# Performance work log

Hardware: AMD Instinct MI355X
Metric: run time of the kernel (lower is better)

The kernel has to match this reference:

```python
import jax, jax.numpy as jnp
import numpy as np

B, N, NODE_DIM, D, H, K, VP = 64, 1024, 8, 128, 4, 16, 128
FF = 512


def _layernorm(x, g, b):
    m = jnp.mean(x, axis=-1, keepdims=True)
    v = jnp.var(x, axis=-1, keepdims=True)
    return (x - m) * jax.lax.rsqrt(v + 1e-5) * g + b


def setup_inputs() -> dict:
    key = jax.random.key(0)
    kit = iter(jax.random.split(key, 64))

    def w(*shape):
        fan_in = shape[-2] if len(shape) >= 2 else shape[-1]
        return jax.random.normal(next(kit), shape, jnp.float32) / np.sqrt(fan_in)

    return dict(
        node_inputs=jax.random.normal(next(kit), (B, N, NODE_DIM), jnp.float32),
        node_padding_mask=jnp.zeros((B, 1, N), jnp.bool_),
        current_index=jax.random.randint(next(kit), (B, 1, 1), 0, N),
        viewpoints=jax.random.randint(next(kit), (B, VP, 1), 0, N),
        viewpoint_padding_mask=jnp.zeros((B, 1, VP), jnp.bool_),
        adj_list=jax.random.randint(next(kit), (B, N, K), 0, N),
        W_init=w(NODE_DIM, D), b_init=jnp.zeros((D,), jnp.float32),
        gcn_W=w(4, D, D), gcn_b=jnp.zeros((4, D), jnp.float32),
        tc_fc_W=w(D, D), tc_fc_b=jnp.zeros((D,), jnp.float32),
        tc_ln1_g=jnp.ones((D,), jnp.float32), tc_ln1_b=jnp.zeros((D,), jnp.float32),
        Wq=w(D, H * D), bq=jnp.zeros((H * D,), jnp.float32),
        Wk=w(D, H * D), bk=jnp.zeros((H * D,), jnp.float32),
        Wv=w(D, H * D), bv=jnp.zeros((H * D,), jnp.float32),
        tc_ln2_g=jnp.ones((D,), jnp.float32), tc_ln2_b=jnp.zeros((D,), jnp.float32),
        sg_fc_W=w(D, D), sg_fc_b=jnp.zeros((D,), jnp.float32),
        dec_Wq=w(D, D), dec_Wk=w(D, D), dec_Wv=w(D, D), dec_Wo=w(D, D),
        dec_ln1_g=jnp.ones((D,), jnp.float32), dec_ln1_b=jnp.zeros((D,), jnp.float32),
        ff_W1=w(D, FF), ff_b1=jnp.zeros((FF,), jnp.float32),
        ff_W2=w(FF, D), ff_b2=jnp.zeros((D,), jnp.float32),
        dec_ln2_g=jnp.ones((D,), jnp.float32), dec_ln2_b=jnp.zeros((D,), jnp.float32),
        q_W=w(3 * D, 1), q_b=jnp.zeros((1,), jnp.float32),
    )


def _forward(node_inputs, node_padding_mask, current_index, viewpoints, viewpoint_padding_mask, adj_list,
             W_init, b_init, gcn_W, gcn_b, tc_fc_W, tc_fc_b, tc_ln1_g, tc_ln1_b,
             Wq, bq, Wk, bk, Wv, bv, tc_ln2_g, tc_ln2_b, sg_fc_W, sg_fc_b,
             dec_Wq, dec_Wk, dec_Wv, dec_Wo, dec_ln1_g, dec_ln1_b,
             ff_W1, ff_b1, ff_W2, ff_b2, dec_ln2_g, dec_ln2_b, q_W, q_b):
    Bb, Nn, nd = node_inputs.shape
    d = W_init.shape[1]
    nH = Wq.shape[1] // d  # SGFormer attention heads (per-head dim = d)
    BN = Bb * Nn
    # ---- initial embedding + batched block-diagonal sparse edges (prepare_batch_data) ----
    x0 = node_inputs.reshape(BN, nd) @ W_init + b_init
    offset = (jnp.arange(Bb) * Nn)[:, None, None]
    valid = adj_list >= 0
    row = (jnp.broadcast_to(jnp.arange(Nn)[None, :, None], adj_list.shape) + offset).reshape(-1)
    col = (jnp.where(valid, adj_list, 0) + offset).reshape(-1)
    ew = valid.reshape(-1).astype(x0.dtype)
    deg = jax.ops.segment_sum(ew, row, num_segments=BN) + 1.0  # +1 self-loop
    dinv = jax.lax.rsqrt(deg)
    enorm = (dinv[row] * dinv[col] * ew)[:, None]

    def gcn_conv(h, W, b):
        hw = h @ W
        agg = jax.ops.segment_sum(enorm * hw[col], row, num_segments=BN)
        return agg + hw / deg[:, None] + b  # self-loop term D^-1 * x W

    h = x0
    n_layers = gcn_W.shape[0]
    for i in range(n_layers):
        h = gcn_conv(h, gcn_W[i], gcn_b[i])
        if i < n_layers - 1:
            h = jax.nn.relu(h)
    gnn_out = h
    # ---- SGFormer TransConv: fc -> LN -> relu, then linear global attention over all BN nodes ----
    z0 = jax.nn.relu(_layernorm(x0 @ tc_fc_W + tc_fc_b, tc_ln1_g, tc_ln1_b))
    q = (z0 @ Wq + bq).reshape(BN, nH, d)
    k = (z0 @ Wk + bk).reshape(BN, nH, d)
    v = (z0 @ Wv + bv).reshape(BN, nH, d)
    qs = q / jnp.linalg.norm(q)  # global Frobenius norm, as in SGFormer
    ks = k / jnp.linalg.norm(k)
    Nf = jnp.asarray(BN, x0.dtype)
    kvs = jnp.einsum('lhm,lhd->hmd', ks, v)
    num = jnp.einsum('nhm,hmd->nhd', qs, kvs) + Nf * v
    den = jnp.einsum('nhm,hm->nh', qs, ks.sum(axis=0))[..., None] + Nf
    attn = (num / den).mean(axis=1)  # mean over heads -> [BN, d]
    z = jax.nn.relu(_layernorm(0.5 * attn + 0.5 * z0, tc_ln2_g, tc_ln2_b))  # alpha=0.5 residual
    enhanced = ((0.8 * gnn_out + 0.2 * z) @ sg_fc_W + sg_fc_b).reshape(Bb, Nn, d)  # graph_weight=0.8
    # ---- decoder: gather current node, masked cross-attention to all nodes ----
    cur = jnp.take_along_axis(enhanced, jnp.broadcast_to(current_index, (Bb, 1, d)), axis=1)
    dH = 4
    dk = d // dH
    qd = (cur @ dec_Wq).reshape(Bb, 1, dH, dk).transpose(0, 2, 1, 3)
    kd = (enhanced @ dec_Wk).reshape(Bb, Nn, dH, dk).transpose(0, 2, 1, 3)
    vd = (enhanced @ dec_Wv).reshape(Bb, Nn, dH, dk).transpose(0, 2, 1, 3)
    scores = jnp.einsum('bhqe,bhne->bhqn', qd, kd) / np.sqrt(dk).astype(np.float32)
    scores = jnp.where(node_padding_mask[:, None, :, :], -1e9, scores)
    wts = jax.nn.softmax(scores, axis=-1)
    att = jnp.einsum('bhqn,bhne->bhqe', wts, vd).transpose(0, 2, 1, 3).reshape(Bb, 1, d) @ dec_Wo
    t = _layernorm(cur + att, dec_ln1_g, dec_ln1_b)
    glob = _layernorm(t + jax.nn.relu(t @ ff_W1 + ff_b1) @ ff_W2 + ff_b2, dec_ln2_g, dec_ln2_b)
    # ---- Q head: gather viewpoints, concat(global, current, viewpoint) -> Linear(3d, 1) ----
    Vp = viewpoints.shape[1]
    vp = jnp.take_along_axis(enhanced, jnp.broadcast_to(viewpoints, (Bb, Vp, d)), axis=1)
    cs = jnp.concatenate([glob, cur], axis=-1)  # [B,1,2d]
    af = jnp.concatenate([jnp.broadcast_to(cs, (Bb, Vp, 2 * d)), vp], axis=-1)
    return af @ q_W + q_b  # [B, Vp, 1]


def reference(node_inputs, node_padding_mask, current_index, viewpoints, viewpoint_padding_mask, adj_list,
              W_init, b_init, gcn_W, gcn_b, tc_fc_W, tc_fc_b, tc_ln1_g, tc_ln1_b,
              Wq, bq, Wk, bk, Wv, bv, tc_ln2_g, tc_ln2_b, sg_fc_W, sg_fc_b,
              dec_Wq, dec_Wk, dec_Wv, dec_Wo, dec_ln1_g, dec_ln1_b,
              ff_W1, ff_b1, ff_W2, ff_b2, dec_ln2_g, dec_ln2_b, q_W, q_b):
    return _forward(node_inputs, node_padding_mask, current_index, viewpoints, viewpoint_padding_mask, adj_list,
                    W_init, b_init, gcn_W, gcn_b, tc_fc_W, tc_fc_b, tc_ln1_g, tc_ln1_b,
                    Wq, bq, Wk, bk, Wv, bv, tc_ln2_g, tc_ln2_b, sg_fc_W, sg_fc_b,
                    dec_Wq, dec_Wk, dec_Wv, dec_Wo, dec_ln1_g, dec_ln1_b,
                    ff_W1, ff_b1, ff_W2, ff_b2, dec_ln2_g, dec_ln2_b, q_W, q_b)
```

## Files before the change

### kernel.cpp

```cpp
#include <hip/hip_runtime.h>

#define BNn 65536L

typedef unsigned short u16;
typedef unsigned int u32;
typedef __attribute__((ext_vector_type(8))) short short8;
typedef __attribute__((ext_vector_type(4))) float f32x4;

__device__ inline u16 f2b(float f){ u32 u = __float_as_uint(f); u32 r = (u + 0x7fffu + ((u>>16)&1u))>>16; return (u16)r; }
__device__ inline float b2f(u16 b){ return __uint_as_float(((u32)b)<<16); }

__global__ __launch_bounds__(256) void k_init(const float* __restrict__ gcnW, const float* __restrict__ tcW,
                       const float* __restrict__ sgW, const float* __restrict__ dKW,
                       const float* __restrict__ dVW,
                       const float* __restrict__ Wq, const float* __restrict__ Wk, const float* __restrict__ Wv,
                       const float* __restrict__ in, const float* __restrict__ Wi, const float* __restrict__ bi,
                       const int* __restrict__ adj, float* __restrict__ dinv,
                       u16* __restrict__ wts, float* __restrict__ SqSkz, u16* __restrict__ x0) {
  __shared__ u16 sT[64 * 136];
  __shared__ float Ws[1024];
  __shared__ float bs[128];
  __shared__ float ins[256];
  int bid = blockIdx.x, t = threadIdx.x;
  if (bid < 41) {
// ... 185 lines not shown
      int valid = a >= 0;
      int cc = (valid ? a : 0) + bb;
      cols[q] = cc;
      enq[q] = valid ? din * dinv[cc] : 0.0f;
    }
    float acc[32];
    {
      const u16* hr = h + n * 128 + seg * 32;
      uint4 v0 = *(const uint4*)(hr), v1 = *(const uint4*)(hr + 8), v2 = *(const uint4*)(hr + 16), v3 = *(const uint4*)(hr + 24);
      const u16* pv = (const u16*)&v0;
#pragma unroll
      for (int i = 0; i < 8; i++) acc[i] = b2f(pv[i]) * d2v;
      pv = (const u16*)&v1;
#pragma unroll
      for (int i = 0; i < 8; i++) acc[8 + i] = b2f(pv[i]) * d2v;
      pv = (const u16*)&v2;
#pragma unroll
      for (int i = 0; i < 8; i++) acc[16 + i] = b2f(pv[i]) * d2v;
      pv = (const u16*)&v3;
#pragma unroll
      for (int i = 0; i < 8; i++) acc[24 + i] = b2f(pv[i]) * d2v;
    }
#pragma unroll
    for (int j = 0; j < 16; j++) {
      int src = (lane & 60) | (j >> 2);
      int cc = __shfl(cols[j & 3], src);
      float e = __shfl(enq[j & 3], src);
      const u16* nb = h + (long)cc * 128 + seg * 32;
      uint4 v0 = *(const uint4*)(nb), v1 = *(const uint4*)(nb + 8), v2 = *(const uint4*)(nb + 16), v3 = *(const uint4*)(nb + 24);
      const u16* pv = (const u16*)&v0;
#pragma unroll
      for (int i = 0; i < 8; i++) acc[i] += e * b2f(pv[i]);
      pv = (const u16*)&v1;
#pragma unroll
      for (int i = 0; i < 8; i++) acc[8 + i] += e * b2f(pv[i]);
      pv = (const u16*)&v2;
#pragma unroll
      for (int i = 0; i < 8; i++) acc[16 + i] += e * b2f(pv[i]);
      pv = (const u16*)&v3;
#pragma unroll
      for (int i = 0; i < 8; i++) acc[24 + i] += e * b2f(pv[i]);
    }
    u16 ob[32];
#pragma unroll
    for (int i = 0; i < 32; i++) ob[i] = f2b(acc[i]);
    uint4* o4 = (uint4*)(sA + row * 132 + seg * 32);
    uint4* s4 = (uint4*)ob;
#pragma unroll
    for (int i = 0; i < 4; i++) o4[i] = s4[i];
  }
  __syncthreads();
  int wave = t >> 6, m = lane & 15, g = lane >> 4;
  const u16* aB = sA + (wave * 16 + m) * 132 + g * 8;
  short8 a[4];
#pragma unroll
  for (int s = 0; s < 4; s++) a[s] = *(const short8*)(aB + s * 32);
  f32x4 acc[8];
#pragma unroll
  for (int c = 0; c < 8; c++) {
    float bc = gb[c * 16 + m];
    acc[c] = (f32x4){bc, bc, bc, bc};
  }
#pragma unroll
  for (int s = 0; s < 4; s++) {
#pragma unroll
    for (int c = 0; c < 8; c++) {
      short8 bb = *(const short8*)(sW + (c * 16 + m) * 132 + g * 8 + s * 32);
      acc[c] = __builtin_amdgcn_mfma_f32_16x16x32_bf16(a[s], bb, acc[c], 0, 0, 0);
    }
  }
#pragma unroll
  for (int c = 0; c < 8; c++) {
    int col = c * 16 + m;
#pragma unroll
    for (int r = 0; r < 4; r++) {
      float y = acc[c][r];
      if (relu) y = fmaxf(y, 0.f);
      out[(n0 + wave * 16 + g * 4 + r) * 128 + col] = f2b(y);
    }
  }
}

__global__ __launch_bounds__(256) void k_gram(const u16* __restrict__ z0T,
                                              float* __restrict__ Gpart, float* __restrict__ zsum) {
  __shared__ u16 sZT[128 * 264];
  int t = threadIdx.x;
  int wave = t >> 6, lane = t & 63, m = lane & 15, g = lane >> 4;
  f32x4 acc[2][8];
#pragma unroll
  for (int i = 0; i < 2; i++)
#pragma unroll
    for (int c = 0; c < 8; c++) acc[i][c] = (f32x4){0.f, 0.f, 0.f, 0.f};
  float zs = 0.f;
  for (int sl = 0; sl < 2; sl++) {
    long k0 = (long)(blockIdx.x * 2 + sl) * 256;
    __syncthreads();
#pragma unroll
    for (int i = 0; i < 16; i++) {
      int idx = t + i * 256; int mm = idx >> 5, ch = idx & 31;
      *(float4*)(sZT + mm * 264 + ch * 8) = *(const float4*)(z0T + (long)mm * BNn + k0 + ch * 8);
    }
    __syncthreads();
#pragma unroll
    for (int kk = 0; kk < 8; kk++) {
      short8 a0 = *(const short8*)(sZT + (wave * 32 + m) * 264 + kk * 32 + g * 8);
      short8 a1 = *(const short8*)(sZT + (wave * 32 + 16 + m) * 264 + kk * 32 + g * 8);
#pragma unroll
      for (int c = 0; c < 8; c++) {
        short8 bb = *(const short8*)(sZT + (c * 16 + m) * 264 + kk * 32 + g * 8);
        acc[0][c] = __builtin_amdgcn_mfma_f32_16x16x32_bf16(a0, bb, acc[0][c], 0, 0, 0);
        acc[1][c] = __builtin_amdgcn_mfma_f32_16x16x32_bf16(a1, bb, acc[1][c], 0, 0, 0);
      }
    }
    if (t < 128) {
      float s = 0.f;
      for (int j = 0; j < 256; j++) s += b2f(sZT[t * 264 + j]);
      zs += s;
    }
  }
  if (t < 128) atomicAdd(&zsum[t], zs);
  float* P = Gpart + (long)blockIdx.x * 16384 + wave * 4096;
#pragma unroll
  for (int i = 0; i < 2; i++)
#pragma unroll
    for (int c = 0; c < 8; c++)
      *(f32x4*)(P + (i * 8 + c) * 256 + lane * 4) = acc[i][c];
}

__global__ void k_gram_red(const float* __restrict__ Gpart, float* __restrict__ G) {
  int o = blockIdx.x * 256 + threadIdx.x;
  float s = 0.f;
  for (int b = 0; b < 128; b++) s += Gpart[(long)b * 16384 + o];
  int wave = o >> 12, rem = o & 4095;
  int ic = rem >> 8, i = ic >> 3, c = ic & 7;
  int rem2 = rem & 255, lane = rem2 >> 2, q = rem2 & 3;
  int m = lane & 15, g = lane >> 4;
  int mi = wave * 32 + i * 16 + g * 4 + q;
  int mj = c * 16 + m;
  G[mi * 128 + mj] = s;
}

__global__ __launch_bounds__(256) void k_statskvs(const float* __restrict__ Wq, const float* __restrict__ bq,
                                                  const float* __restrict__ Wk, const float* __restrict__ bk,
                                                  const float* __restrict__ Wv, const float* __restrict__ bv,
                                                  const float* __restrict__ G, const float* __restrict__ zsum,
                                                  float* __restrict__ ksum,
                                                  float* __restrict__ Sq, float* __restrict__ Sk,
                                                  u16* __restrict__ kvsT) {
  int t = threadIdx.x;
  int blk = blockIdx.x;
  if (blk < 2) {
    int c = blk * 256 + t;
    float s = 0.f;
    for (int i = 0; i < 128; i++) s += Wk[i * 512 + c] * zsum[i];
    ksum[c] = s + 65536.0f * bk[c];
    return;
  }
  if (blk < 130) {
    __shared__ float wcol[128];
    __shared__ float red[256];
    int bi = blk - 2;
    int isK = bi >> 6;
    const float* W = isK ? Wk : Wq;
    const float* bb = isK ? bk : bq;
    float* S = isK ? Sk : Sq;
    int c0 = (bi & 63) * 8;
    float tot = 0.f;
    for (int cc = 0; cc < 8; cc++) {
      int c = c0 + cc;
      __syncthreads();
      if (t < 128) wcol[t] = W[t * 512 + c];
      __syncthreads();
      float v = 0.f;
      if (t < 128) {
        float uu = 0.f;
        for (int j = 0; j < 128; j++) uu += G[t * 128 + j] * wcol[j];
        v = uu * wcol[t] + 2.0f * bb[c] * wcol[t] * zsum[t];
      }
      red[t] = v;
      __syncthreads();
      for (int o = 128; o > 0; o >>= 1) { if (t < o) red[t] += red[t + o]; __syncthreads(); }
      if (t == 0) tot += red[0] + 65536.0f * bb[c] * bb[c];
    }
    if (t == 0) atomicAdd(S, tot);
    return;
  }
  {
    __shared__ float wv8[128][8];
    __shared__ float U[128][8];
    __shared__ float zv[8];
    int bi = blk - 130;
    int h = bi >> 4, dg = bi & 15;
    if (t < 128) {
#pragma unroll
      for (int dd = 0; dd < 8; dd++) wv8[t][dd] = Wv[t * 512 + h * 128 + dg * 8 + dd];
    }
    __syncthreads();
    {
      int i = t & 127, du = t >> 7;
      float a0 = 0.f, a1 = 0.f, a2 = 0.f, a3 = 0.f;
      for (int j = 0; j < 128; j++) {
        float gg = G[i * 128 + j];
        a0 += gg * wv8[j][du * 4 + 0]; a1 += gg * wv8[j][du * 4 + 1];
        a2 += gg * wv8[j][du * 4 + 2]; a3 += gg * wv8[j][du * 4 + 3];
      }
      U[i][du * 4 + 0] = a0; U[i][du * 4 + 1] = a1; U[i][du * 4 + 2] = a2; U[i][du * 4 + 3] = a3;
    }
    if (t < 8) {
      float s = 0.f;
      for (int i = 0; i < 128; i++) s += zsum[i] * wv8[i][t];
      zv[t] = s;
    }
    __syncthreads();
    {
      int m = t & 127, du = t >> 7;
      int colk = h * 128 + m;
      float bkm = bk[colk];
      float a[4] = {0.f, 0.f, 0.f, 0.f};
      float wkzs = 0.f;
      for (int i = 0; i < 128; i++) {
        float wk = Wk[i * 512 + colk];
        wkzs += wk * zsum[i];
#pragma unroll
        for (int q = 0; q < 4; q++) a[q] += wk * U[i][du * 4 + q];
      }
#pragma unroll
      for (int q = 0; q < 4; q++) {
        int dd = du * 4 + q;
        int cold = h * 128 + dg * 8 + dd;
        float val = a[q] + wkzs * bv[cold] + bkm * zv[dd] + 65536.0f * bkm * bv[cold];
        kvsT[h * 16384 + (dg * 8 + dd) * 128 + m] = f2b(val);
      }
    }
  }
}

__global__ __launch_bounds__(256) void k_prepB(const float* __restrict__ Wq, const float* __restrict__ bq,
                                               const float* __restrict__ Wv, const float* __restrict__ bv,
                                               const u16* __restrict__ kvsT, const float* __restrict__ ksum,
                                               const float* __restrict__ SqSk,
                                               u16* __restrict__ Bmat, float* __restrict__ cAv,
                                               u16* __restrict__ U16, float* __restrict__ consts) {
  __shared__ float kvr[8][128];
  int t = threadIdx.x;
  int h = blockIdx.x >> 4, dg = blockIdx.x & 15;
  float inv = rsqrtf(SqSk[0] * SqSk[1]);
  for (int i = t; i < 1024; i += 256) {
    int dl = i >> 7, m = i & 127;
    kvr[dl][m] = b2f(kvsT[h * 16384 + (dg * 8 + dl) * 128 + m]);
  }
  __syncthreads();
  {
    int k = t & 127, du = t >> 7;
    const float* wqr = Wq + k * 512 + h * 128;
    float acc[4] = {0.f, 0.f, 0.f, 0.f};
    for (int m = 0; m < 128; m++) {
      float w = wqr[m];
#pragma unroll
      for (int q = 0; q < 4; q++) acc[q] += w * kvr[du * 4 + q][m];
    }
#pragma unroll
    for (int q = 0; q < 4; q++) {
      int dd = dg * 8 + du * 4 + q;
      float mv = acc[q] * inv + 65536.0f * Wv[k * 512 + h * 128 + dd];
      Bmat[((long)h * 128 + dd) * 128 + k] = f2b(mv);
    }
  }
  if (t < 8) {
    float s = 0.f;
    for (int m = 0; m < 128; m++) s += bq[h * 128 + m] * kvr[t][m];
    cAv[h * 128 + dg * 8 + t] = s * inv + 65536.0f * bv[h * 128 + dg * 8 + t];
  }
  if (dg == 0) {
    if (t < 128) {
      float s = 0.f;
      for (int m = 0; m < 128; m++) s += Wq[t * 512 + h * 128 + m] * ksum[h * 128 + m];
      U16[h * 128 + t] = f2b(s * inv);
    } else if (t == 128) {
      float s = 0.f;
      for (int m = 0; m < 128; m++) s += bq[h * 128 + m] * ksum[h * 128 + m];
      consts[h] = s * inv + 65536.0f;
    }
    if (h == 0) {
      for (int i = t; i < 1536; i += 256) U16[512 + i] = 0;
    }
  }
}

__global__ __launch_bounds__(512) void k_numfuse(const u16* __restrict__ z0, const u16* __restrict__ gnn,
                                                 const u16* __restrict__ Bmat,
                                                 const float* __restrict__ cAv, const u16* __restrict__ U16,
                                                 const float* __restrict__ consts,
                                                 const float* __restrict__ g2, const float* __restrict__ b2,
                                                 const u16* __restrict__ wsg, const float* __restrict__ sgb,
                                                 u16* __restrict__ enh) {
  __shared__ u16 sA[128 * 132];
  __shared__ u16 sB[128 * 132];
  __shared__ float rden[512];
  __shared__ float caL[512];
  int t = threadIdx.x;
  long n0 = (long)blockIdx.x * 128;
  int wave = t >> 6, lane = t & 63, m = lane & 15, g = lane >> 4;
  u16* myA = sA + wave * 16 * 132;
  {
    const u16* zg = z0 + (n0 + wave * 16) * 128;
#pragma unroll
    for (int i = 0; i < 4; i++) {
      int idx = lane + i * 64; int row = idx >> 4, ch = idx & 15;
      *(float4*)(myA + row * 132 + ch * 8) = *(const float4*)(zg + row * 128 + ch * 8);
    }
  }
  caL[t] = cAv[t & 511];
  const u16* aB = sA + (wave * 16 + m) * 132 + g * 8;
  short8 a[4];
#pragma unroll
  for (int s = 0; s < 4; s++) a[s] = *(const short8*)(aB + s * 32);
  {
    f32x4 accd = (f32x4){0.f, 0.f, 0.f, 0.f};
#pragma unroll
    for (int s = 0; s < 4; s++) {
      short8 ub = *(const short8*)(U16 + m * 128 + g * 8 + s * 32);
      accd = __builtin_amdgcn_mfma_f32_16x16x32_bf16(a[s], ub, accd, 0, 0, 0);
    }
    if (m < 4) {
      float ch = consts[m];
#pragma unroll
      for (int r = 0; r < 4; r++)
        rden[(wave * 16 + g * 4 + r) * 4 + m] = 1.0f / (accd[r] + ch);
    }
  }
  f32x4 attn[8];
#pragma unroll
  for (int c = 0; c < 8; c++) attn[c] = (f32x4){0.f, 0.f, 0.f, 0.f};
  for (int h = 0; h < 4; h++) {
    __syncthreads();
    {
      const u16* src = Bmat + (long)h * 16384;
#pragma unroll
      for (int i = 0; i < 4; i++) {
        int idx = t + i * 512; int row = idx >> 4, ch = idx & 15;
        *(float4*)(sB + row * 132 + ch * 8) = *(const float4*)(src + row * 128 + ch * 8);
      }
    }
    __syncthreads();
    f32x4 acc[8];
#pragma unroll
    for (int c = 0; c < 8; c++) {
      float ca = caL[h * 128 + c * 16 + m];
      acc[c] = (f32x4){ca, ca, ca, ca};
    }
#pragma unroll
    for (int s = 0; s < 4; s++) {
#pragma unroll
      for (int c = 0; c < 8; c++) {
        short8 bb = *(const short8*)(sB + (c * 16 + m) * 132 + g * 8 + s * 32);
        acc[c] = __builtin_amdgcn_mfma_f32_16x16x32_bf16(a[s], bb, acc[c], 0, 0, 0);
      }
    }
#pragma unroll
    for (int c = 0; c < 8; c++)
#pragma unroll
      for (int r = 0; r < 4; r++)
        attn[c][r] += acc[c][r] * rden[(wave * 16 + g * 4 + r) * 4 + h];
  }
  float y[8][4];
#pragma unroll
  for (int c = 0; c < 8; c++)
#pragma unroll
    for (int r = 0; r < 4; r++)
      y[c][r] = 0.125f * attn[c][r] + 0.5f * b2f(sA[(wave * 16 + g * 4 + r) * 132 + c * 16 + m]);
  float mu[4], rstd[4];
#pragma unroll
  for (int r = 0; r < 4; r++) {
    float s1 = 0.f, s2 = 0.f;
#pragma unroll
    for (int c = 0; c < 8; c++) { float v = y[c][r]; s1 += v; s2 += v * v; }
#pragma unroll
    for (int mask = 1; mask < 16; mask <<= 1) { s1 += __shfl_xor(s1, mask); s2 += __shfl_xor(s2, mask); }
    float mm2 = s1 * (1.f / 128.f);
    mu[r] = mm2; rstd[r] = rsqrtf(s2 * (1.f / 128.f) - mm2 * mm2 + 1e-5f);
  }
  {
    const u16* gg = gnn + (n0 + wave * 16) * 128;
#pragma unroll
    for (int i = 0; i < 4; i++) {
      int idx = lane + i * 64; int row = idx >> 4, ch = idx & 15;
      *(float4*)(myA + row * 132 + ch * 8) = *(const float4*)(gg + row * 128 + ch * 8);
    }
  }
#pragma unroll
  for (int c = 0; c < 8; c++) {
    int d = c * 16 + m;
    float ggc = g2[d], bbc = b2[d];
#pragma unroll
    for (int r = 0; r < 4; r++) {
      int loc = (wave * 16 + g * 4 + r) * 132 + d;
      float zr = fmaxf((y[c][r] - mu[r]) * rstd[r] * ggc + bbc, 0.f);
      sA[loc] = f2b(0.8f * b2f(sA[loc]) + 0.2f * zr);
    }
  }
  __syncthreads();
  {
#pragma unroll
    for (int i = 0; i < 4; i++) {
      int idx = t + i * 512; int row = idx >> 4, ch = idx & 15;
      *(float4*)(sB + row * 132 + ch * 8) = *(const float4*)(wsg + row * 128 + ch * 8);
    }
  }
  __syncthreads();
  short8 ap[4];
#pragma unroll
  for (int s = 0; s < 4; s++) ap[s] = *(const short8*)(aB + s * 32);
  f32x4 acc2[8];
#pragma unroll
  for (int c = 0; c < 8; c++) {
    float bc = sgb[c * 16 + m];
    acc2[c] = (f32x4){bc, bc, bc, bc};
  }
#pragma unroll
  for (int s = 0; s < 4; s++) {
#pragma unroll
    for (int c = 0; c < 8; c++) {
      short8 bb = *(const short8*)(sB + (c * 16 + m) * 132 + g * 8 + s * 32);
      acc2[c] = __builtin_amdgcn_mfma_f32_16x16x32_bf16(ap[s], bb, acc2[c], 0, 0, 0);
    }
  }
#pragma unroll
  for (int c = 0; c < 8; c++) {
    int d = c * 16 + m;
#pragma unroll
    for (int r = 0; r < 4; r++)
      enh[(n0 + wave * 16 + g * 4 + r) * 128 + d] = f2b(acc2[c][r]);
  }
}

__global__ __launch_bounds__(128) void k_dq(const u16* __restrict__ enh, const int* __restrict__ cidx,
                                            const float* __restrict__ dWq, const float* __restrict__ dWk,
                                            float* __restrict__ cur_ws, float* __restrict__ qt_ws) {
  __shared__ float cur[128], qd[128];
  int b = blockIdx.x, t = threadIdx.x;
  int ci = cidx[b];
  cur[t] = b2f(enh[((long)b * 1024 + ci) * 128 + t]);
  cur_ws[b * 128 + t] = cur[t];
  __syncthreads();
  {
    float s = 0.f;
    for (int k = 0; k < 128; k++) s += cur[k] * dWq[k * 128 + t];
    qd[t] = s;
  }
  __syncthreads();
#pragma unroll
  for (int h = 0; h < 4; h++) {
    float s = 0.f;
#pragma unroll
    for (int c = 0; c < 32; c++) s += dWk[t * 128 + h * 32 + c] * qd[h * 32 + c];
    qt_ws[(b * 4 + h) * 128 + t] = s;
  }
}

__global__ __launch_bounds__(128) void k_dsc(const u16* __restrict__ enh, const float* __restrict__ qt_ws,
                                             float* __restrict__ sc_ws) {
  __shared__ float qtL[4][128];
  int b = blockIdx.y, chunk = blockIdx.x, t = threadIdx.x;
#pragma unroll
  for (int h = 0; h < 4; h++) qtL[h][t] = qt_ws[(b * 4 + h) * 128 + t];
  __syncthreads();
  long n = (long)b * 1024 + chunk * 128 + t;
  const u16* er = enh + n * 128;
  float s0 = 0.f, s1 = 0.f, s2 = 0.f, s3 = 0.f;
#pragma unroll
  for (int i8 = 0; i8 < 16; i8++) {
    short8 ev = *(const short8*)(er + i8 * 8);
#pragma unroll
    for (int j = 0; j < 8; j++) {
      float e = b2f((u16)ev[j]);
      int k = i8 * 8 + j;
      s0 += e * qtL[0][k]; s1 += e * qtL[1][k]; s2 += e * qtL[2][k]; s3 += e * qtL[3][k];
    }
  }
  const float scale = 0.17677669529663687f;
  long o = ((long)(b * 4) << 10) + chunk * 128 + t;
  sc_ws[o] = s0 * scale;
  sc_ws[o + 1024] = s1 * scale;
  sc_ws[o + 2048] = s2 * scale;
  sc_ws[o + 3072] = s3 * scale;
}

__global__ __launch_bounds__(256) void k_dsm(float* __restrict__ sc_ws, float* __restrict__ dinv_ws) {
  __shared__ float red[256];
  __shared__ float bm;
  int bh = blockIdx.x, t = threadIdx.x;
  float* sc = sc_ws + ((long)bh << 10);
  f32x4 v = *(f32x4*)(sc + t * 4);
  float mx = fmaxf(fmaxf(v[0], v[1]), fmaxf(v[2], v[3]));
  red[t] = mx;
  __syncthreads();
  for (int o = 128; o > 0; o >>= 1) { if (t < o) red[t] = fmaxf(red[t], red[t + o]); __syncthreads(); }
  if (t == 0) bm = red[0];
  __syncthreads();
  float mv = bm;
  v[0] = __expf(v[0] - mv); v[1] = __expf(v[1] - mv); v[2] = __expf(v[2] - mv); v[3] = __expf(v[3] - mv);
  *(f32x4*)(sc + t * 4) = v;
  red[t] = v[0] + v[1] + v[2] + v[3];
  __syncthreads();
  for (int o = 128; o > 0; o >>= 1) { if (t < o) red[t] += red[t + o]; __syncthreads(); }
  if (t == 0) dinv_ws[bh] = 1.0f / red[0];
}

__global__ __launch_bounds__(256) void k_dpv(const u16* __restrict__ enh, const float* __restrict__ sc_ws,
                                             float* __restrict__ pv_ws) {
  __shared__ float pL[4][128];
  __shared__ float pvL[4][4][128];
  int b = blockIdx.y, chunk = blockIdx.x, t = threadIdx.x;
  long n0 = (long)b * 1024 + chunk * 128;
  if (t < 128) {
#pragma unroll
    for (int h = 0; h < 4; h++) pL[h][t] = sc_ws[((long)(b * 4 + h) << 10) + chunk * 128 + t];
  }
  __syncthreads();
  int seg = t & 15, part = t >> 4;
  float acc[4][8];
#pragma unroll
  for (int h = 0; h < 4; h++)
#pragma unroll
    for (int j = 0; j < 8; j++) acc[h][j] = 0.f;
  for (int i = 0; i < 8; i++) {
    int n = part * 8 + i;
    short8 e8 = *(const short8*)(enh + (n0 + n) * 128 + seg * 8);
    float p0 = pL[0][n], p1 = pL[1][n], p2 = pL[2][n], p3 = pL[3][n];
#pragma unroll
    for (int j = 0; j < 8; j++) {
      float e = b2f((u16)e8[j]);
      acc[0][j] += p0 * e; acc[1][j] += p1 * e; acc[2][j] += p2 * e; acc[3][j] += p3 * e;
    }
  }
#pragma unroll
  for (int h = 0; h < 4; h++)
#pragma unroll
    for (int j = 0; j < 8; j++) {
      acc[h][j] += __shfl_xor(acc[h][j], 16);
      acc[h][j] += __shfl_xor(acc[h][j], 32);
    }
  int wave = t >> 6, lane = t & 63;
  if (lane < 16) {
#pragma unroll
    for (int h = 0; h < 4; h++)
#pragma unroll
      for (int j = 0; j < 8; j++) pvL[wave][h][seg * 8 + j] = acc[h][j];
  }
  __syncthreads();
  if (t < 128) {
#pragma unroll
    for (int h = 0; h < 4; h++) {
      float s = pvL[0][h][t] + pvL[1][h][t] + pvL[2][h][t] + pvL[3][h][t];
      pv_ws[(((long)(b * 8 + chunk)) * 4 + h) * 128 + t] = s;
    }
  }
}

__global__ __launch_bounds__(256) void k_dfin(const u16* __restrict__ enh, const int* __restrict__ vps,
                                              const float* __restrict__ cur_ws, const float* __restrict__ pv_ws,
                                              const float* __restrict__ dinv_ws,
                                              const float* __restrict__ dWv, const float* __restrict__ dWo,
                                              const float* __restrict__ ln1g, const float* __restrict__ ln1b,
                                              const float* __restrict__ fW1, const float* __restrict__ fb1,
                                              const float* __restrict__ fW2, const float* __restrict__ fb2,
                                              const float* __restrict__ ln2g, const float* __restrict__ ln2b,
                                              const float* __restrict__ qW, const float* __restrict__ qb,
                                              float* __restrict__ out) {
  __shared__ float cur[128], sH[4][128], att[128], tn[128], tv[128], f1[512], red[256], glob[128];
  __shared__ float mu_s, rs_s, base_s;
  int b = blockIdx.x, t = threadIdx.x;
  const u16* eb = enh + (long)b * 1024 * 128;
  if (t < 128) {
    cur[t] = cur_ws[b * 128 + t];
#pragma unroll
    for (int h = 0; h < 4; h++) {
      float s = 0.f;
#pragma unroll
      for (int c = 0; c < 8; c++) s += pv_ws[(((long)(b * 8 + c)) * 4 + h) * 128 + t];
      sH[h][t] = s;
    }
  }
  __syncthreads();
  if (t < 128) {
    int h = t >> 5, e = t & 31;
    float s = 0.f;
    for (int k = 0; k < 128; k++) s += sH[h][k] * dWv[k * 128 + h * 32 + e];
    att[t] = s * dinv_ws[b * 4 + h];
  }
  __syncthreads();
  if (t < 128) {
    float s = 0.f;
    for (int k = 0; k < 128; k++) s += att[k] * dWo[k * 128 + t];
    tv[t] = cur[t] + s;
  }
  {
    __syncthreads();
    float v = (t < 128) ? tv[t] : 0.f;
    red[t] = v; __syncthreads();
    for (int o = 128; o > 0; o >>= 1) { if (t < o) red[t] += red[t + o]; __syncthreads(); }
    float s1 = red[0];
    __syncthreads();
    red[t] = v * v; __syncthreads();
    for (int o = 128; o > 0; o >>= 1) { if (t < o) red[t] += red[t + o]; __syncthreads(); }
    if (t == 0) {
      float mm = s1 / 128.0f;
      mu_s = mm; rs_s = rsqrtf(red[0] / 128.0f - mm * mm + 1e-5f);
    }
    __syncthreads();
    if (t < 128) tn[t] = (tv[t] - mu_s) * rs_s * ln1g[t] + ln1b[t];
    __syncthreads();
  }
#pragma unroll
  for (int i = 0; i < 2; i++) {
    int c = t + 256 * i;
    float s = fb1[c];
    for (int k = 0; k < 128; k++) s += tn[k] * fW1[k * 512 + c];
    f1[c] = fmaxf(s, 0.0f);
  }
  __syncthreads();
  if (t < 128) {
    float s = fb2[t];
    for (int k = 0; k < 512; k++) s += f1[k] * fW2[k * 128 + t];
    tv[t] = tn[t] + s;
  }
  {
    __syncthreads();
    float v = (t < 128) ? tv[t] : 0.f;
    red[t] = v; __syncthreads();
    for (int o = 128; o > 0; o >>= 1) { if (t < o) red[t] += red[t + o]; __syncthreads(); }
    float s1 = red[0];
    __syncthreads();
    red[t] = v * v; __syncthreads();
    for (int o = 128; o > 0; o >>= 1) { if (t < o) red[t] += red[t + o]; __syncthreads(); }
    if (t == 0) {
      float mm = s1 / 128.0f;
      mu_s = mm; rs_s = rsqrtf(red[0] / 128.0f - mm * mm + 1e-5f);
    }
    __syncthreads();
    if (t < 128) glob[t] = (tv[t] - mu_s) * rs_s * ln2g[t] + ln2b[t];
    __syncthreads();
  }
  red[t] = (t < 128 ? glob[t] : cur[t - 128]) * qW[t];
  __syncthreads();
  for (int o = 128; o > 0; o >>= 1) { if (t < o) red[t] += red[t + o]; __syncthreads(); }
  if (t == 0) base_s = red[0] + qb[0];
  __syncthreads();
  if (t < 128) {
    int vi = vps[b * 128 + t];
    const u16* er = eb + (long)vi * 128;
    float s = 0.f;
#pragma unroll
    for (int i8 = 0; i8 < 16; i8++) {
      short8 ev = *(const short8*)(er + i8 * 8);
#pragma unroll
      for (int j = 0; j < 8; j++) s += b2f((u16)ev[j]) * qW[256 + i8 * 8 + j];
    }
    out[b * 128 + t] = base_s + s;
  }
}

extern "C" void kernel_launch(void* const* d_in, const int* in_sizes, int n_in,
                              void* d_out, int out_size, void* d_ws, size_t ws_size,
                              hipStream_t stream) {
  const float* node_in = (const float*)d_in[0];
  const int* cur_idx   = (const int*)d_in[2];
  const int* vps       = (const int*)d_in[3];
  const int* adj       = (const int*)d_in[5];
  const float* W_init  = (const float*)d_in[6];
  const float* b_init  = (const float*)d_in[7];
  const float* gcn_W   = (const float*)d_in[8];
  const float* gcn_b   = (const float*)d_in[9];
  const float* tc_fc_W = (const float*)d_in[10];
  const float* tc_fc_b = (const float*)d_in[11];
  const float* ln1g    = (const float*)d_in[12];
  const float* ln1b    = (const float*)d_in[13];
  const float* Wq      = (const float*)d_in[14];
  const float* bq      = (const float*)d_in[15];
  const float* Wk      = (const float*)d_in[16];
  const float* bk      = (const float*)d_in[17];
  const float* Wv      = (const float*)d_in[18];
  const float* bv      = (const float*)d_in[19];
  const float* ln2g    = (const float*)d_in[20];
  const float* ln2b    = (const float*)d_in[21];
  const float* sg_W    = (const float*)d_in[22];
  const float* sg_b    = (const float*)d_in[23];
  const float* dWq     = (const float*)d_in[24];
  const float* dWk     = (const float*)d_in[25];
  const float* dWv     = (const float*)d_in[26];
  const float* dWo     = (const float*)d_in[27];
  const float* dln1g   = (const float*)d_in[28];
  const float* dln1b   = (const float*)d_in[29];
  const float* fW1     = (const float*)d_in[30];
  const float* fb1     = (const float*)d_in[31];
  const float* fW2     = (const float*)d_in[32];
  const float* fb2     = (const float*)d_in[33];
  const float* dln2g   = (const float*)d_in[34];
  const float* dln2b   = (const float*)d_in[35];
  const float* qW      = (const float*)d_in[36];
  const float* qb      = (const float*)d_in[37];

  char* base = (char*)d_ws;
  u16* bufA = (u16*)base;
  u16* bufB = (u16*)(base + 16777216);
  u16* bufC = (u16*)(base + 33554432);
  u16* z0T  = (u16*)(base + 50331648);
  float* Gpart = (float*)(base + 67108864);
  char* sm = base + 83886080;
  u16* kvsT   = (u16*)sm;
  u16* wts    = (u16*)(sm + 131072);
  float* bqkv = (float*)(sm + 131072 + 655360);
  float* ksum = bqkv + 1536;
  float* SqSk = ksum + 512;
  float* zsum = SqSk + 2;
  float* Gm   = zsum + 128;
  float* dinv = Gm + 16384;
  float* cAv  = dinv + BNn;
  float* consts = cAv + 512;
  u16* Bmat = (u16*)(consts + 4);
  u16* U16m = Bmat + 65536;
  float* cur_ws  = Gpart;
  float* qt_ws   = Gpart + 8192;
  float* dinv_ws = Gpart + 40960;
  float* sc_ws   = Gpart + 41216;
  float* pv_ws   = Gpart + 303360;

  k_init<<<2089, 256, 0, stream>>>(gcn_W, tc_fc_W, sg_W, dWk, dWv, Wq, Wk, Wv,
                                   node_in, W_init, b_init, adj, dinv, wts, SqSk, bufA);

  k_gemm<2><<<512, 256, 0, stream>>>(bufA, wts + 4 * 16384, tc_fc_b, ln1g, ln1b, bufB, z0T);

  k_gram<<<128, 256, 0, stream>>>(z0T, Gpart, zsum);
  k_gram_red<<<64, 256, 0, stream>>>(Gpart, Gm);
  k_statskvs<<<194, 256, 0, stream>>>(Wq, bq, Wk, bk, Wv, bv, Gm, zsum, ksum, SqSk, SqSk + 1, kvsT);
  k_prepB<<<64, 256, 0, stream>>>(Wq, bq, Wv, bv, kvsT, ksum, SqSk, Bmat, cAv, U16m, consts);

  k_gcn<<<1024, 256, 0, stream>>>(bufA, wts + 0 * 16384, adj, dinv, gcn_b + 0, bufC, 1);
  k_gcn<<<1024, 256, 0, stream>>>(bufC, wts + 1 * 16384, adj, dinv, gcn_b + 128, bufA, 1);
  k_gcn<<<1024, 256, 0, stream>>>(bufA, wts + 2 * 16384, adj, dinv, gcn_b + 256, bufC, 1);
  k_gcn<<<1024, 256, 0, stream>>>(bufC, wts + 3 * 16384, adj, dinv, gcn_b + 384, bufA, 0);

  k_numfuse<<<512, 512, 0, stream>>>(bufB, bufA, Bmat, cAv, U16m, consts, ln2g, ln2b,
                                     wts + 5 * 16384, sg_b, bufB);

  k_dq<<<64, 128, 0, stream>>>(bufB, cur_idx, dWq, dWk, cur_ws, qt_ws);
  k_dsc<<<dim3(8, 64), 128, 0, stream>>>(bufB, qt_ws, sc_ws);
  k_dsm<<<256, 256, 0, stream>>>(sc_ws, dinv_ws);
  k_dpv<<<dim3(8, 64), 256, 0, stream>>>(bufB, sc_ws, pv_ws);
  k_dfin<<<64, 256, 0, stream>>>(bufB, vps, cur_ws, pv_ws, dinv_ws, dWv, dWo, dln1g, dln1b,
                                 fW1, fb1, fW2, fb2, dln2g, dln2b, qW, qb, (float*)d_out);
}
```

Before: 443.8 us.

## Prefetch next weight tile into registers during MFMA loop in k_numfuse

Register-prefetches the next head's B matrix (and then the sg weight and gnn rows) from global memory while the current head's MFMAs run, so each store to shared memory replaces a synchronous global load. It also hoists the rden reads into registers and raises wave priority around the MFMA blocks. This is meant to hide global-load latency in one kernel of a multi-kernel pipeline, at the cost of extra registers and a different barrier pattern.

```diff
diff --git a/kernel.cpp b/kernel.cpp
--- a/kernel.cpp
+++ b/kernel.cpp
@@ -511,6 +511,12 @@
   long n0 = (long)blockIdx.x * 128;
   int wave = t >> 6, lane = t & 63, m = lane & 15, g = lane >> 4;
   u16* myA = sA + wave * 16 * 132;
+  float4 st[4];
+  int srow[4], sch[4];
+#pragma unroll
+  for (int i = 0; i < 4; i++) { int idx = t + i * 512; srow[i] = idx >> 4; sch[i] = idx & 15; }
+#pragma unroll
+  for (int i = 0; i < 4; i++) st[i] = *(const float4*)(Bmat + (long)srow[i] * 128 + sch[i] * 8);
   {
     const u16* zg = z0 + (n0 + wave * 16) * 128;
 #pragma unroll
@@ -519,7 +525,7 @@
       *(float4*)(myA + row * 132 + ch * 8) = *(const float4*)(zg + row * 128 + ch * 8);
     }
   }
-  caL[t] = cAv[t & 511];
+  caL[t] = cAv[t];
   const u16* aB = sA + (wave * 16 + m) * 132 + g * 8;
   short8 a[4];
 #pragma unroll
@@ -538,26 +544,24 @@
         rden[(wave * 16 + g * 4 + r) * 4 + m] = 1.0f / (accd[r] + ch);
     }
   }
+#pragma unroll
+  for (int i = 0; i < 4; i++) *(float4*)(sB + srow[i] * 132 + sch[i] * 8) = st[i];
+  __syncthreads();
   f32x4 attn[8];
 #pragma unroll
   for (int c = 0; c < 8; c++) attn[c] = (f32x4){0.f, 0.f, 0.f, 0.f};
+#pragma unroll
   for (int h = 0; h < 4; h++) {
-    __syncthreads();
-    {
-      const u16* src = Bmat + (long)h * 16384;
-#pragma unroll
-      for (int i = 0; i < 4; i++) {
-        int idx = t + i * 512; int row = idx >> 4, ch = idx & 15;
-        *(float4*)(sB + row * 132 + ch * 8) = *(const float4*)(src + row * 128 + ch * 8);
-      }
-    }
-    __syncthreads();
+    const u16* nsrc = (h < 3) ? (Bmat + (long)(h + 1) * 16384) : wsg;
+#pragma unroll
+    for (int i = 0; i < 4; i++) st[i] = *(const float4*)(nsrc + (long)srow[i] * 128 + sch[i] * 8);
     f32x4 acc[8];
 #pragma unroll
     for (int c = 0; c < 8; c++) {
       float ca = caL[h * 128 + c * 16 + m];
       acc[c] = (f32x4){ca, ca, ca, ca};
     }
+    __builtin_amdgcn_s_setprio(1);
 #pragma unroll
     for (int s = 0; s < 4; s++) {
 #pragma unroll
@@ -566,11 +570,26 @@
         acc[c] = __builtin_amdgcn_mfma_f32_16x16x32_bf16(a[s], bb, acc[c], 0, 0, 0);
       }
     }
+    __builtin_amdgcn_s_setprio(0);
+    float rd[4];
+#pragma unroll
+    for (int r = 0; r < 4; r++) rd[r] = rden[(wave * 16 + g * 4 + r) * 4 + h];
 #pragma unroll
     for (int c = 0; c < 8; c++)
 #pragma unroll
-      for (int r = 0; r < 4; r++)
-        attn[c][r] += acc[c][r] * rden[(wave * 16 + g * 4 + r) * 4 + h];
+      for (int r = 0; r < 4; r++) attn[c][r] += acc[c][r] * rd[r];
+    __syncthreads();
+#pragma unroll
+    for (int i = 0; i < 4; i++) *(float4*)(sB + srow[i] * 132 + sch[i] * 8) = st[i];
+    if (h == 3) {
+      const u16* gg = gnn + (n0 + wave * 16) * 128;
+#pragma unroll
+      for (int i = 0; i < 4; i++) {
+        int idx = lane + i * 64; int row = idx >> 4, ch = idx & 15;
+        st[i] = *(const float4*)(gg + row * 128 + ch * 8);
+      }
+    }
+    __syncthreads();
   }
   float y[8][4];
 #pragma unroll
@@ -589,13 +608,10 @@
     float mm2 = s1 * (1.f / 128.f);
     mu[r] = mm2; rstd[r] = rsqrtf(s2 * (1.f / 128.f) - mm2 * mm2 + 1e-5f);
   }
-  {
-    const u16* gg = gnn + (n0 + wave * 16) * 128;
-#pragma unroll
-    for (int i = 0; i < 4; i++) {
-      int idx = lane + i * 64; int row = idx >> 4, ch = idx & 15;
-      *(float4*)(myA + row * 132 + ch * 8) = *(const float4*)(gg + row * 128 + ch * 8);
-    }
+#pragma unroll
+  for (int i = 0; i < 4; i++) {
+    int idx = lane + i * 64; int row = idx >> 4, ch = idx & 15;
+    *(float4*)(myA + row * 132 + ch * 8) = st[i];
   }
 #pragma unroll
   for (int c = 0; c < 8; c++) {
@@ -608,15 +624,6 @@
       sA[loc] = f2b(0.8f * b2f(sA[loc]) + 0.2f * zr);
     }
   }
-  __syncthreads();
-  {
-#pragma unroll
-    for (int i = 0; i < 4; i++) {
-      int idx = t + i * 512; int row = idx >> 4, ch = idx & 15;
-      *(float4*)(sB + row * 132 + ch * 8) = *(const float4*)(wsg + row * 128 + ch * 8);
-    }
-  }
-  __syncthreads();
   short8 ap[4];
 #pragma unroll
   for (int s = 0; s < 4; s++) ap[s] = *(const short8*)(aB + s * 32);
@@ -626,6 +633,7 @@
     float bc = sgb[c * 16 + m];
     acc2[c] = (f32x4){bc, bc, bc, bc};
   }
+  __builtin_amdgcn_s_setprio(1);
 #pragma unroll
   for (int s = 0; s < 4; s++) {
 #pragma unroll
@@ -634,6 +642,7 @@
       acc2[c] = __builtin_amdgcn_mfma_f32_16x16x32_bf16(ap[s], bb, acc2[c], 0, 0, 0);
     }
   }
+  __builtin_amdgcn_s_setprio(0);
 #pragma unroll
   for (int c = 0; c < 8; c++) {
     int d = c * 16 + m;
```

Result: slower. 465.8 us (+5.0%).

## Fuse decoder attention kernels into a single per-batch kernel

Applied to the files above, without the earlier changes.

Merges the query projection, score, softmax, probability-weighted sum and final decoder stages into one kernel with one block per batch element. Scores and softmax now stay in shared memory, removing several launches and global workspace round-trips. In exchange, the two passes over the embeddings run on only 64 blocks, which reduces memory-level parallelism.

```diff
diff --git a/kernel.cpp b/kernel.cpp
--- a/kernel.cpp
+++ b/kernel.cpp
@@ -643,160 +643,132 @@
   }
 }
 
-__global__ __launch_bounds__(128) void k_dq(const u16* __restrict__ enh, const int* __restrict__ cidx,
-                                            const float* __restrict__ dWq, const float* __restrict__ dWk,
-                                            float* __restrict__ cur_ws, float* __restrict__ qt_ws) {
-  __shared__ float cur[128], qd[128];
+__global__ __launch_bounds__(256) void k_dec(const u16* __restrict__ enh, const int* __restrict__ cidx,
+                                             const int* __restrict__ vps,
+                                             const float* __restrict__ dWq, const float* __restrict__ dWk,
+                                             const float* __restrict__ dWv, const float* __restrict__ dWo,
+                                             const float* __restrict__ ln1g, const float* __restrict__ ln1b,
+                                             const float* __restrict__ fW1, const float* __restrict__ fb1,
+                                             const float* __restrict__ fW2, const float* __restrict__ fb2,
+                                             const float* __restrict__ ln2g, const float* __restrict__ ln2b,
+                                             const float* __restrict__ qW, const float* __restrict__ qb,
+                                             float* __restrict__ out) {
+  __shared__ float cur[128], qd[128], qtL[4][128];
+  __shared__ float scL[4][1024];
+  __shared__ float mxs[4], dinvs[4];
+  __shared__ float pvL[4][4][128], sH[4][128];
+  __shared__ float att[128], tn[128], tv[128], f1[512], red[256], glob[128];
+  __shared__ float mu_s, rs_s, base_s;
   int b = blockIdx.x, t = threadIdx.x;
-  int ci = cidx[b];
-  cur[t] = b2f(enh[((long)b * 1024 + ci) * 128 + t]);
-  cur_ws[b * 128 + t] = cur[t];
-  __syncthreads();
-  {
+  int wave = t >> 6, lane = t & 63;
+  const u16* eb = enh + (long)b * 1024 * 128;
+  if (t < 128) {
+    int ci = cidx[b];
+    cur[t] = b2f(eb[(long)ci * 128 + t]);
+  }
+  __syncthreads();
+  if (t < 128) {
     float s = 0.f;
     for (int k = 0; k < 128; k++) s += cur[k] * dWq[k * 128 + t];
     qd[t] = s;
   }
   __syncthreads();
-#pragma unroll
-  for (int h = 0; h < 4; h++) {
-    float s = 0.f;
-#pragma unroll
-    for (int c = 0; c < 32; c++) s += dWk[t * 128 + h * 32 + c] * qd[h * 32 + c];
-    qt_ws[(b * 4 + h) * 128 + t] = s;
-  }
-}
-
-__global__ __launch_bounds__(128) void k_dsc(const u16* __restrict__ enh, const float* __restrict__ qt_ws,
-                                             float* __restrict__ sc_ws) {
-  __shared__ float qtL[4][128];
-  int b = blockIdx.y, chunk = blockIdx.x, t = threadIdx.x;
-#pragma unroll
-  for (int h = 0; h < 4; h++) qtL[h][t] = qt_ws[(b * 4 + h) * 128 + t];
-  __syncthreads();
-  long n = (long)b * 1024 + chunk * 128 + t;
-  const u16* er = enh + n * 128;
-  float s0 = 0.f, s1 = 0.f, s2 = 0.f, s3 = 0.f;
-#pragma unroll
-  for (int i8 = 0; i8 < 16; i8++) {
-    short8 ev = *(const short8*)(er + i8 * 8);
-#pragma unroll
-    for (int j = 0; j < 8; j++) {
-      float e = b2f((u16)ev[j]);
-      int k = i8 * 8 + j;
-      s0 += e * qtL[0][k]; s1 += e * qtL[1][k]; s2 += e * qtL[2][k]; s3 += e * qtL[3][k];
-    }
-  }
-  const float scale = 0.17677669529663687f;
-  long o = ((long)(b * 4) << 10) + chunk * 128 + t;
-  sc_ws[o] = s0 * scale;
-  sc_ws[o + 1024] = s1 * scale;
-  sc_ws[o + 2048] = s2 * scale;
-  sc_ws[o + 3072] = s3 * scale;
-}
-
-__global__ __launch_bounds__(256) void k_dsm(float* __restrict__ sc_ws, float* __restrict__ dinv_ws) {
-  __shared__ float red[256];
-  __shared__ float bm;
-  int bh = blockIdx.x, t = threadIdx.x;
-  float* sc = sc_ws + ((long)bh << 10);
-  f32x4 v = *(f32x4*)(sc + t * 4);
-  float mx = fmaxf(fmaxf(v[0], v[1]), fmaxf(v[2], v[3]));
-  red[t] = mx;
-  __syncthreads();
-  for (int o = 128; o > 0; o >>= 1) { if (t < o) red[t] = fmaxf(red[t], red[t + o]); __syncthreads(); }
-  if (t == 0) bm = red[0];
-  __syncthreads();
-  float mv = bm;
-  v[0] = __expf(v[0] - mv); v[1] = __expf(v[1] - mv); v[2] = __expf(v[2] - mv); v[3] = __expf(v[3] - mv);
-  *(f32x4*)(sc + t * 4) = v;
-  red[t] = v[0] + v[1] + v[2] + v[3];
-  __syncthreads();
-  for (int o = 128; o > 0; o >>= 1) { if (t < o) red[t] += red[t + o]; __syncthreads(); }
-  if (t == 0) dinv_ws[bh] = 1.0f / red[0];
-}
-
-__global__ __launch_bounds__(256) void k_dpv(const u16* __restrict__ enh, const float* __restrict__ sc_ws,
-                                             float* __restrict__ pv_ws) {
-  __shared__ float pL[4][128];
-  __shared__ float pvL[4][4][128];
-  int b = blockIdx.y, chunk = blockIdx.x, t = threadIdx.x;
-  long n0 = (long)b * 1024 + chunk * 128;
   if (t < 128) {
-#pragma unroll
-    for (int h = 0; h < 4; h++) pL[h][t] = sc_ws[((long)(b * 4 + h) << 10) + chunk * 128 + t];
-  }
-  __syncthreads();
-  int seg = t & 15, part = t >> 4;
-  float acc[4][8];
-#pragma unroll
-  for (int h = 0; h < 4; h++)
-#pragma unroll
-    for (int j = 0; j < 8; j++) acc[h][j] = 0.f;
-  for (int i = 0; i < 8; i++) {
-    int n = part * 8 + i;
-    short8 e8 = *(const short8*)(enh + (n0 + n) * 128 + seg * 8);
-    float p0 = pL[0][n], p1 = pL[1][n], p2 = pL[2][n], p3 = pL[3][n];
-#pragma unroll
-    for (int j = 0; j < 8; j++) {
-      float e = b2f((u16)e8[j]);
-      acc[0][j] += p0 * e; acc[1][j] += p1 * e; acc[2][j] += p2 * e; acc[3][j] += p3 * e;
-    }
-  }
-#pragma unroll
-  for (int h = 0; h < 4; h++)
-#pragma unroll
-    for (int j = 0; j < 8; j++) {
-      acc[h][j] += __shfl_xor(acc[h][j], 16);
-      acc[h][j] += __shfl_xor(acc[h][j], 32);
-    }
-  int wave = t >> 6, lane = t & 63;
-  if (lane < 16) {
-#pragma unroll
-    for (int h = 0; h < 4; h++)
-#pragma unroll
-      for (int j = 0; j < 8; j++) pvL[wave][h][seg * 8 + j] = acc[h][j];
-  }
-  __syncthreads();
-  if (t < 128) {
-#pragma unroll
-    for (int h = 0; h < 4; h++) {
-      float s = pvL[0][h][t] + pvL[1][h][t] + pvL[2][h][t] + pvL[3][h][t];
-      pv_ws[(((long)(b * 8 + chunk)) * 4 + h) * 128 + t] = s;
-    }
-  }
-}
-
-__global__ __launch_bounds__(256) void k_dfin(const u16* __restrict__ enh, const int* __restrict__ vps,
-                                              const float* __restrict__ cur_ws, const float* __restrict__ pv_ws,
-                                              const float* __restrict__ dinv_ws,
-                                              const float* __restrict__ dWv, const float* __restrict__ dWo,
-                                              const float* __restrict__ ln1g, const float* __restrict__ ln1b,
-                                              const float* __restrict__ fW1, const float* __restrict__ fb1,
-                                              const float* __restrict__ fW2, const float* __restrict__ fb2,
-                                              const float* __restrict__ ln2g, const float* __restrict__ ln2b,
-                                              const float* __restrict__ qW, const float* __restrict__ qb,
-                                              float* __restrict__ out) {
-  __shared__ float cur[128], sH[4][128], att[128], tn[128], tv[128], f1[512], red[256], glob[128];
-  __shared__ float mu_s, rs_s, base_s;
-  int b = blockIdx.x, t = threadIdx.x;
-  const u16* eb = enh + (long)b * 1024 * 128;
-  if (t < 128) {
-    cur[t] = cur_ws[b * 128 + t];
 #pragma unroll
     for (int h = 0; h < 4; h++) {
       float s = 0.f;
 #pragma unroll
-      for (int c = 0; c < 8; c++) s += pv_ws[(((long)(b * 8 + c)) * 4 + h) * 128 + t];
-      sH[h][t] = s;
-    }
+      for (int c = 0; c < 32; c++) s += dWk[t * 128 + h * 32 + c] * qd[h * 32 + c];
+      qtL[h][t] = s;
+    }
+  }
+  __syncthreads();
+  const float scale = 0.17677669529663687f;
+#pragma unroll
+  for (int i = 0; i < 4; i++) {
+    int n = t * 4 + i;
+    const u16* er = eb + (long)n * 128;
+    float s0 = 0.f, s1 = 0.f, s2 = 0.f, s3 = 0.f;
+#pragma unroll
+    for (int i8 = 0; i8 < 16; i8++) {
+      short8 ev = *(const short8*)(er + i8 * 8);
+#pragma unroll
+      for (int j = 0; j < 8; j++) {
+        float e = b2f((u16)ev[j]);
+        int k = i8 * 8 + j;
+        s0 += e * qtL[0][k]; s1 += e * qtL[1][k]; s2 += e * qtL[2][k]; s3 += e * qtL[3][k];
+      }
+    }
+    scL[0][n] = s0 * scale; scL[1][n] = s1 * scale; scL[2][n] = s2 * scale; scL[3][n] = s3 * scale;
+  }
+  __syncthreads();
+  {
+    float mx = -3.0e38f;
+    for (int k = lane; k < 1024; k += 64) mx = fmaxf(mx, scL[wave][k]);
+#pragma unroll
+    for (int msk = 1; msk < 64; msk <<= 1) mx = fmaxf(mx, __shfl_xor(mx, msk));
+    if (lane == 0) mxs[wave] = mx;
+  }
+  __syncthreads();
+#pragma unroll
+  for (int h = 0; h < 4; h++) {
+    f32x4 v = *(f32x4*)&scL[h][t * 4];
+    float mv = mxs[h];
+    v[0] = __expf(v[0] - mv); v[1] = __expf(v[1] - mv); v[2] = __expf(v[2] - mv); v[3] = __expf(v[3] - mv);
+    *(f32x4*)&scL[h][t * 4] = v;
+  }
+  __syncthreads();
+  {
+    float sm = 0.f;
+    for (int k = lane; k < 1024; k += 64) sm += scL[wave][k];
+#pragma unroll
+    for (int msk = 1; msk < 64; msk <<= 1) sm += __shfl_xor(sm, msk);
+    if (lane == 0) dinvs[wave] = 1.0f / sm;
+  }
+  __syncthreads();
+  {
+    int seg = t & 15, part = t >> 4;
+    float acc[4][8];
+#pragma unroll
+    for (int h = 0; h < 4; h++)
+#pragma unroll
+      for (int j = 0; j < 8; j++) acc[h][j] = 0.f;
+    for (int i = 0; i < 64; i++) {
+      int n = part * 64 + i;
+      short8 e8 = *(const short8*)(eb + (long)n * 128 + seg * 8);
+      float p0 = scL[0][n], p1 = scL[1][n], p2 = scL[2][n], p3 = scL[3][n];
+#pragma unroll
+      for (int j = 0; j < 8; j++) {
+        float e = b2f((u16)e8[j]);
+        acc[0][j] += p0 * e; acc[1][j] += p1 * e; acc[2][j] += p2 * e; acc[3][j] += p3 * e;
+      }
+    }
+#pragma unroll
+    for (int h = 0; h < 4; h++)
+#pragma unroll
+      for (int j = 0; j < 8; j++) {
+        acc[h][j] += __shfl_xor(acc[h][j], 16);
+        acc[h][j] += __shfl_xor(acc[h][j], 32);
+      }
+    if (lane < 16) {
+#pragma unroll
+      for (int h = 0; h < 4; h++)
+#pragma unroll
+        for (int j = 0; j < 8; j++) pvL[wave][h][seg * 8 + j] = acc[h][j];
+    }
+  }
+  __syncthreads();
+  if (t < 128) {
+#pragma unroll
+    for (int h = 0; h < 4; h++)
+      sH[h][t] = pvL[0][h][t] + pvL[1][h][t] + pvL[2][h][t] + pvL[3][h][t];
   }
   __syncthreads();
   if (t < 128) {
     int h = t >> 5, e = t & 31;
     float s = 0.f;
     for (int k = 0; k < 128; k++) s += sH[h][k] * dWv[k * 128 + h * 32 + e];
-    att[t] = s * dinv_ws[b * 4 + h];
+    att[t] = s * dinvs[h];
   }
   __syncthreads();
   if (t < 128) {
@@ -929,11 +901,6 @@
   float* consts = cAv + 512;
   u16* Bmat = (u16*)(consts + 4);
   u16* U16m = Bmat + 65536;
-  float* cur_ws  = Gpart;
-  float* qt_ws   = Gpart + 8192;
-  float* dinv_ws = Gpart + 40960;
-  float* sc_ws   = Gpart + 41216;
-  float* pv_ws   = Gpart + 303360;
 
   k_init<<<2089, 256, 0, stream>>>(gcn_W, tc_fc_W, sg_W, dWk, dWv, Wq, Wk, Wv,
                                    node_in, W_init, b_init, adj, dinv, wts, SqSk, bufA);
@@ -953,10 +920,6 @@
   k_numfuse<<<512, 512, 0, stream>>>(bufB, bufA, Bmat, cAv, U16m, consts, ln2g, ln2b,
                                      wts + 5 * 16384, sg_b, bufB);
 
-  k_dq<<<64, 128, 0, stream>>>(bufB, cur_idx, dWq, dWk, cur_ws, qt_ws);
-  k_dsc<<<dim3(8, 64), 128, 0, stream>>>(bufB, qt_ws, sc_ws);
-  k_dsm<<<256, 256, 0, stream>>>(sc_ws, dinv_ws);
-  k_dpv<<<dim3(8, 64), 256, 0, stream>>>(bufB, sc_ws, pv_ws);
-  k_dfin<<<64, 256, 0, stream>>>(bufB, vps, cur_ws, pv_ws, dinv_ws, dWv, dWo, dln1g, dln1b,
-                                 fW1, fb1, fW2, fb2, dln2g, dln2b, qW, qb, (float*)d_out);
+  k_dec<<<64, 256, 0, stream>>>(bufB, cur_idx, vps, dWq, dWk, dWv, dWo, dln1g, dln1b,
+                                fW1, fb1, fW2, fb2, dln2g, dln2b, qW, qb, (float*)d_out);
 }
```

New measurement: 446.4 us. About the same (+0.6%).
